# Performance work log

Hardware: AMD Instinct MI355X
Metric: run time of the kernel (lower is better)

The kernel has to match this reference:

```python
import jax, jax.numpy as jnp
import numpy as np

B, L, D = 16, 1024, 256  # batch, c_len == q_len (required by the expand/add in the source), 2*d_model


def mask_logits(x, m):
    # Faithful to the source's (unusual) masking: x*m + x*(1-m)*1e30
    return x * m + x * (1.0 - m) * 1e30


def setup_inputs() -> dict:
    key = jax.random.key(0)
    k = jax.random.split(key, 7)
    c = jax.random.normal(k[0], (B, L, D), dtype=jnp.float32)
    q = jax.random.normal(k[1], (B, L, D), dtype=jnp.float32)
    c_mask = jnp.ones((B, 1, L), dtype=jnp.float32)
    q_mask = jnp.ones((B, 1, L), dtype=jnp.float32)
    # Learned parameters (nn.Parameter zeros in the source; random here so the test is non-degenerate)
    c_weight = jax.random.normal(k[2], (D, 1), dtype=jnp.float32) * 0.05
    q_weight = jax.random.normal(k[3], (D, 1), dtype=jnp.float32) * 0.05
    cq_weight = jax.random.normal(k[4], (1, 1, D), dtype=jnp.float32) * 0.05
    bias = jnp.zeros((1,), dtype=jnp.float32)
    return {"c": c, "q": q, "c_mask": c_mask, "q_mask": q_mask,
            "c_weight": c_weight, "q_weight": q_weight,
            "cq_weight": cq_weight, "bias": bias}


def reference(c, q, c_mask, q_mask, c_weight, q_weight, cq_weight, bias):
    # Dropout treated as identity (inference) for a deterministic reference.
    s0 = jnp.matmul(c, c_weight)                      # [B, L, 1] -> broadcasts over q_len
    s1 = jnp.swapaxes(jnp.matmul(c, q_weight), 1, 2)  # [B, 1, L] (source uses c here, not q)
    s2 = jnp.einsum('bid,bjd->bij', c * cq_weight, q) # [B, L, L]
    S = s0 + s1 + s2 + bias                           # trilinear similarity
    S1 = jax.nn.softmax(mask_logits(S, q_mask), axis=-1)              # [B, Lc, Lq]
    C2Q = jnp.matmul(S1, q)                                           # [B, Lc, D]
    # torch F.softmax with no dim on a 3D tensor defaults to dim=0 (legacy behavior) -> axis=0
    S2 = jax.nn.softmax(mask_logits(jnp.swapaxes(S, 1, 2), c_mask), axis=0)  # [B, Lq, Lc]
    S2 = jnp.matmul(S1, S2)                                           # [B, Lc, Lc]
    Q2C = jnp.matmul(S2, c)                                           # [B, Lc, D]
    # torch.cat default dim=0 -> [4B, Lc, D]
    return jnp.concatenate((c, C2Q, c * C2Q, c * Q2C), axis=0)
```

## Files before the change

kernel.cpp:

```cpp
#include <hip/hip_runtime.h>

typedef __bf16 bf16;
typedef _Float16 f16;
typedef __attribute__((ext_vector_type(8))) __bf16 bf16x8;
typedef __attribute__((ext_vector_type(4))) __bf16 bf16x4;
typedef __attribute__((ext_vector_type(8))) _Float16 f16x8;
typedef __attribute__((ext_vector_type(4))) _Float16 f16x4;
typedef __attribute__((ext_vector_type(4))) float f32x4;

constexpr int Bn = 16, Ln = 1024, Dn = 256;

__device__ __forceinline__ float maskf(float m) { return m + (1.0f - m) * 1e30f; }

__device__ __forceinline__ void gload16(const void* g, void* l) {
  __builtin_amdgcn_global_load_lds((const __attribute__((address_space(1))) void*)g,
                                   (__attribute__((address_space(3))) void*)l, 16, 0, 0);
}

#define VMCNT(N) asm volatile("s_waitcnt vmcnt(" #N ")" ::: "memory")
#define LGKM0 asm volatile("s_waitcnt lgkmcnt(0)" ::: "memory")
#define BARR                                  \
  do {                                        \
    asm volatile("" ::: "memory");            \
    __builtin_amdgcn_s_barrier();             \
    asm volatile("" ::: "memory");            \
  } while (0)

__device__ __forceinline__ void stage512(const bf16* __restrict__ G, int ldg, int k0,
                                         bf16* L, int tid, int wid) {
#pragma unroll
  for (int p = 0; p < 2; ++p) {
    int u = tid + (p << 9);
    int row = u >> 3, s = u & 7;
    int kk = ((s ^ (row & 7)) << 3);
    gload16(G + (size_t)row * ldg + k0 + kk, L + ((p << 9) + (wid << 6)) * 8);
  }
}

__device__ __forceinline__ const bf16* swzp(const bf16* L, int row, int slot) {
  return L + row * 64 + ((slot ^ (row & 7)) << 3);
}

__global__ __launch_bounds__(256) void k_prep2(
    const float* __restrict__ c, const float* __restrict__ q,
    const float* __restrict__ cw, const float* __restrict__ qw,
    const float* __restrict__ cqw, bf16* __restrict__ cm, bf16* __restrict__ qb,
    bf16* __restrict__ cT, bf16* __restrict__ qT,
    float* __restrict__ s0, float* __restrict__ s1) {
  __shared__ __align__(16) bf16 tc[32][264];
  __shared__ __align__(16) bf16 tq[32][264];
  int blk = blockIdx.x;
  int b = blk >> 5;
  int l0 = (blk & 31) << 5;
  int t = threadIdx.x;
  int rl = t >> 3;
  int c0 = (t & 7) << 5;
  int grow = b * Ln + l0 + rl;
  size_t base = (size_t)grow * Dn + c0;
  float4 cv[8], qv[8];
#pragma unroll
  for (int k = 0; k < 8; ++k) {
    cv[k] = *(const float4*)&c[base + k * 4];
    qv[k] = *(const float4*)&q[base + k * 4];
  }
  float d0 = 0.f, d1 = 0.f;
#pragma unroll
  for (int k = 0; k < 8; ++k) {
    float4 w = *(const float4*)&cw[c0 + k * 4];
    float4 u = *(const float4*)&qw[c0 + k * 4];
    d0 += cv[k].x * w.x + cv[k].y * w.y + cv[k].z * w.z + cv[k].w * w.w;
    d1 += cv[k].x * u.x + cv[k].y * u.y + cv[k].z * u.z + cv[k].w * u.w;
  }
  d0 += __shfl_xor(d0, 1); d0 += __shfl_xor(d0, 2); d0 += __shfl_xor(d0, 4);
  d1 += __shfl_xor(d1, 1); d1 += __shfl_xor(d1, 2); d1 += __shfl_xor(d1, 4);
  if ((t & 7) == 0) { s0[grow] = d0; s1[grow] = d1; }
#pragma unroll
  for (int k2 = 0; k2 < 4; ++k2) {
    float4 m0 = *(const float4*)&cqw[c0 + k2 * 8];
    float4 m1 = *(const float4*)&cqw[c0 + k2 * 8 + 4];
    bf16x8 vm, vq, vc;
#pragma unroll
    for (int e = 0; e < 8; ++e) {
      float cvv = ((const float*)&cv[k2 * 2 + (e >> 2)])[e & 3];
      float qvv = ((const float*)&qv[k2 * 2 + (e >> 2)])[e & 3];
      float mw = (e < 4) ? ((const float*)&m0)[e] : ((const float*)&m1)[e - 4];
      vm[e] = (bf16)(cvv * mw);
      vq[e] = (bf16)qvv;
      vc[e] = (bf16)cvv;
    }
    *(bf16x8*)&cm[base + k2 * 8] = vm;
    *(bf16x8*)&qb[base + k2 * 8] = vq;
    *(bf16x8*)&tc[rl][c0 + k2 * 8] = vc;
    *(bf16x8*)&tq[rl][c0 + k2 * 8] = vq;
  }
  __syncthreads();
  int d = t;
  size_t tb = ((size_t)b * Dn + d) * Ln + l0;
  bf16x8 o[4];
#pragma unroll
  for (int j = 0; j < 4; ++j)
#pragma unroll
    for (int e = 0; e < 8; ++e) o[j][e] = tc[j * 8 + e][d];
#pragma unroll
  for (int j = 0; j < 4; ++j) *(bf16x8*)&cT[tb + j * 8] = o[j];
#pragma unroll
  for (int j = 0; j < 4; ++j)
#pragma unroll
    for (int e = 0; e < 8; ++e) o[j][e] = tq[j * 8 + e][d];
#pragma unroll
  for (int j = 0; j < 4; ++j) *(bf16x8*)&qT[tb + j * 8] = o[j];
}

__global__ __launch_bounds__(512) void g_s(const bf16* __restrict__ Am,
                                           const bf16* __restrict__ Bm,
                                           const float* __restrict__ s0,
                                           const float* __restrict__ s1,
                                           const float* __restrict__ bias,
                                           f16* __restrict__ S) {
  __shared__ __align__(16) bf16 lds[2][2 * 128 * 64];
  int f = blockIdx.x;
  int o = (f & 7) * 128 + (f >> 3);
  int bx = o & 7, by = (o >> 3) & 7, b = o >> 6;
  const bf16* Ab = Am + (size_t)b * Ln * Dn + (size_t)by * 128 * Dn;
  const bf16* Bb = Bm + (size_t)b * Ln * Dn + (size_t)bx * 128 * Dn;
  const int tid = threadIdx.x, wid = tid >> 6, lane = tid & 63;
  const int r = lane & 15, h = lane >> 4, wr = wid >> 2, wc = wid & 3;
  f32x4 acc[4][2];
  f32x4 zero = {0.f, 0.f, 0.f, 0.f};
#pragma unroll
  for (int i = 0; i < 4; ++i)
#pragma unroll
    for (int j = 0; j < 2; ++j) acc[i][j] = zero;

  stage512(Ab, Dn, 0, &lds[0][0], tid, wid);
  stage512(Bb, Dn, 0, &lds[0][8192], tid, wid);
  for (int t = 0; t < 4; ++t) {
    int cur = t & 1;
    if (t < 3) {
      stage512(Ab, Dn, (t + 1) * 64, &lds[cur ^ 1][0], tid, wid);
      stage512(Bb, Dn, (t + 1) * 64, &lds[cur ^ 1][8192], tid, wid);
      VMCNT(4);
    } else {
      VMCNT(0);
    }
    BARR;
    const bf16* lA = &lds[cur][0];
    const bf16* lB = &lds[cur][8192];
#pragma unroll
    for (int kk2 = 0; kk2 < 2; ++kk2) {
      int slot = (kk2 << 2) | h;
      bf16x8 av[4], bv[2];
#pragma unroll
      for (int i = 0; i < 4; ++i)
        av[i] = *(const bf16x8*)swzp(lA, (wr << 6) + (i << 4) + r, slot);
#pragma unroll
      for (int j = 0; j < 2; ++j)
        bv[j] = *(const bf16x8*)swzp(lB, (wc << 5) + (j << 4) + r, slot);
#pragma unroll
      for (int i = 0; i < 4; ++i)
#pragma unroll
        for (int j = 0; j < 2; ++j)
          acc[i][j] = __builtin_amdgcn_mfma_f32_16x16x32_bf16(av[i], bv[j], acc[i][j], 0, 0, 0);
    }
    LGKM0; BARR;
  }
  int grow = by * 128 + wr * 64, gcol = bx * 128 + wc * 32;
  float bvv = bias[0];
  size_t sb = (size_t)b * Ln * Ln;
#pragma unroll
  for (int j = 0; j < 2; ++j) {
    int n = gcol + j * 16 + r;
    float v1 = s1[b * Ln + n];
#pragma unroll
    for (int i = 0; i < 4; ++i) {
      int mb = grow + i * 16 + h * 4;
#pragma unroll
      for (int g = 0; g < 4; ++g) {
        float v0 = s0[b * Ln + mb + g];
        S[sb + (size_t)(mb + g) * Ln + n] = (f16)(acc[i][j][g] + v0 + v1 + bvv);
      }
    }
  }
}

__global__ __launch_bounds__(256) void k_sm(const f16* __restrict__ S,
                                            const float* __restrict__ qmask,
                                            const float* __restrict__ cmask,
                                            bf16* __restrict__ P1,
                                            bf16* __restrict__ P2) {
  __shared__ __align__(16) bf16 tile[16][32][36];
  int blk = blockIdx.x;
  int t = threadIdx.x;
  if (blk < 1024) {
    int i0 = (blk >> 5) << 5, j0 = (blk & 31) << 5;
    int ti = t >> 3, tj4 = (t & 7) << 2;
    int i = i0 + ti;
    const f16* Sp = S + (size_t)i * Ln + j0 + tj4;
    float fm[16];
#pragma unroll
    for (int b = 0; b < 16; ++b) fm[b] = maskf(cmask[b * Ln + i]);
    f16x4 u[16];
#pragma unroll
    for (int b = 0; b < 16; ++b) u[b] = *(const f16x4*)(Sp + (size_t)b * Ln * Ln);
    float m[4] = {-3.4e38f, -3.4e38f, -3.4e38f, -3.4e38f};
#pragma unroll
    for (int b = 0; b < 16; ++b)
#pragma unroll
      for (int g = 0; g < 4; ++g) m[g] = fmaxf(m[g], (float)u[b][g] * fm[b]);
    float e[16][4];
    float s[4] = {0.f, 0.f, 0.f, 0.f};
#pragma unroll
    for (int b = 0; b < 16; ++b)
#pragma unroll
      for (int g = 0; g < 4; ++g) {
        e[b][g] = __expf((float)u[b][g] * fm[b] - m[g]);
        s[g] += e[b][g];
      }
#pragma unroll
    for (int g = 0; g < 4; ++g) s[g] = 1.0f / s[g];
#pragma unroll
    for (int b = 0; b < 16; ++b)
#pragma unroll
      for (int g = 0; g < 4; ++g) tile[b][tj4 + g][ti] = (bf16)(e[b][g] * s[g]);
    __syncthreads();
    int jl = t >> 3, i4 = (t & 7) << 2;
#pragma unroll
    for (int b = 0; b < 16; ++b) {
      *(bf16x4*)&P2[((size_t)b * Ln + j0 + jl) * Ln + i0 + i4] =
          *(const bf16x4*)&tile[b][jl][i4];
    }
  } else {
    int row = (blk - 1024) * 4 + (t >> 6);
    int b = row >> 10;
    int lane = t & 63;
    const f16* Sr = S + (size_t)row * Ln;
    const float* qm = qmask + (size_t)b * Ln;
    float v[16];
    float mx = -3.4e38f;
#pragma unroll
    for (int p = 0; p < 2; ++p) {
      f16x8 x = ((const f16x8*)Sr)[lane + (p << 6)];
      float4 m0 = ((const float4*)qm)[(lane + (p << 6)) * 2];
      float4 m1 = ((const float4*)qm)[(lane + (p << 6)) * 2 + 1];
      float mm[8] = {m0.x, m0.y, m0.z, m0.w, m1.x, m1.y, m1.z, m1.w};
#pragma unroll
      for (int e = 0; e < 8; ++e) {
        float xv = (float)x[e] * maskf(mm[e]);
        v[8 * p + e] = xv;
        mx = fmaxf(mx, xv);
      }
    }
#pragma unroll
    for (int off = 32; off; off >>= 1) mx = fmaxf(mx, __shfl_xor(mx, off));
    float sum = 0.f;
#pragma unroll
    for (int k = 0; k < 16; ++k) {
      v[k] = __expf(v[k] - mx);
      sum += v[k];
    }
#pragma unroll
    for (int off = 32; off; off >>= 1) sum += __shfl_xor(sum, off);
    float inv = 1.0f / sum;
    bf16* Pr = P1 + (size_t)row * Ln;
#pragma unroll
    for (int p = 0; p < 2; ++p) {
      bf16x8 o;
#pragma unroll
      for (int e = 0; e < 8; ++e) o[e] = (bf16)(v[8 * p + e] * inv);
      ((bf16x8*)Pr)[lane + (p << 6)] = o;
    }
  }
}

__global__ __launch_bounds__(512) void g_t(const bf16* __restrict__ cT,
                                           const bf16* __restrict__ P2,
                                           bf16* __restrict__ TT) {
  __shared__ __align__(16) bf16 lds[2][2 * 128 * 64];
  int f = blockIdx.x;
  int o = (f & 7) * 32 + (f >> 3);
  int b = o >> 4, md = (o >> 3) & 1, nb = o & 7;
  const bf16* Ab = cT + (size_t)b * Dn * Ln + (size_t)md * 128 * Ln;
  const bf16* Bb = P2 + (size_t)b * Ln * Ln + (size_t)nb * 128 * Ln;
  const int tid = threadIdx.x, wid = tid >> 6, lane = tid & 63;
  const int r = lane & 15, h = lane >> 4, wr = wid >> 2, wc = wid & 3;
  f32x4 acc[4][2];
  f32x4 zero = {0.f, 0.f, 0.f, 0.f};
#pragma unroll
  for (int i = 0; i < 4; ++i)
#pragma unroll
    for (int j = 0; j < 2; ++j) acc[i][j] = zero;

  stage512(Ab, Ln, 0, &lds[0][0], tid, wid);
  stage512(Bb, Ln, 0, &lds[0][8192], tid, wid);
  for (int t = 0; t < 16; ++t) {
    int cur = t & 1;
    if (t < 15) {
      stage512(Ab, Ln, (t + 1) * 64, &lds[cur ^ 1][0], tid, wid);
      stage512(Bb, Ln, (t + 1) * 64, &lds[cur ^ 1][8192], tid, wid);
      VMCNT(4);
    } else {
      VMCNT(0);
    }
    BARR;
    const bf16* lA = &lds[cur][0];
    const bf16* lB = &lds[cur][8192];
#pragma unroll
    for (int kk2 = 0; kk2 < 2; ++kk2) {
      int slot = (kk2 << 2) | h;
      bf16x8 av[4], bv[2];
#pragma unroll
      for (int i = 0; i < 4; ++i)
        av[i] = *(const bf16x8*)swzp(lA, (wr << 6) + (i << 4) + r, slot);
#pragma unroll
      for (int j = 0; j < 2; ++j)
        bv[j] = *(const bf16x8*)swzp(lB, (wc << 5) + (j << 4) + r, slot);
#pragma unroll
      for (int i = 0; i < 4; ++i)
#pragma unroll
        for (int j = 0; j < 2; ++j)
          acc[i][j] = __builtin_amdgcn_mfma_f32_16x16x32_bf16(av[i], bv[j], acc[i][j], 0, 0, 0);
    }
    LGKM0; BARR;
  }
  size_t ob = (size_t)b * Dn * Ln;
  int dbase = md * 128 + wr * 64, cbase = nb * 128 + wc * 32;
#pragma unroll
  for (int i = 0; i < 4; ++i)
#pragma unroll
    for (int j = 0; j < 2; ++j) {
      int n = cbase + j * 16 + r;
#pragma unroll
      for (int g = 0; g < 4; ++g)
        TT[ob + (size_t)(dbase + i * 16 + h * 4 + g) * Ln + n] = (bf16)acc[i][j][g];
    }
}

__global__ __launch_bounds__(512) void g_cq(const bf16* __restrict__ P1,
                                            const bf16* __restrict__ qT,
                                            const bf16* __restrict__ TT,
                                            const float* __restrict__ c,
                                            float* __restrict__ out) {
  __shared__ __align__(16) bf16 lds[2][3 * 128 * 64];
  int f = blockIdx.x;
  int o = (f & 7) * 32 + (f >> 3);
  int b = o >> 4, by = (o >> 1) & 7, bx = o & 1;
  const bf16* Ab = P1 + (size_t)b * Ln * Ln + (size_t)by * 128 * Ln;
  const bf16* B1 = qT + (size_t)b * Dn * Ln + (size_t)bx * 128 * Ln;
  const bf16* B2 = TT + (size_t)b * Dn * Ln + (size_t)bx * 128 * Ln;
  const int tid = threadIdx.x, wid = tid >> 6, lane = tid & 63;
  const int r = lane & 15, h = lane >> 4, wr = wid >> 2, wc = wid & 3;
  f32x4 acc1[4][2], acc2[4][2];
  f32x4 zero = {0.f, 0.f, 0.f, 0.f};
#pragma unroll
  for (int i = 0; i < 4; ++i)
#pragma unroll
    for (int j = 0; j < 2; ++j) { acc1[i][j] = zero; acc2[i][j] = zero; }

  stage512(Ab, Ln, 0, &lds[0][0], tid, wid);
  stage512(B1, Ln, 0, &lds[0][8192], tid, wid);
  stage512(B2, Ln, 0, &lds[0][16384], tid, wid);
  for (int t = 0; t < 16; ++t) {
    int cur = t & 1;
    if (t < 15) {
      stage512(Ab, Ln, (t + 1) * 64, &lds[cur ^ 1][0], tid, wid);
      stage512(B1, Ln, (t + 1) * 64, &lds[cur ^ 1][8192], tid, wid);
      stage512(B2, Ln, (t + 1) * 64, &lds[cur ^ 1][16384], tid, wid);
      VMCNT(6);
    } else {
      VMCNT(0);
    }
    BARR;
    const bf16* lA = &lds[cur][0];
    const bf16* lB1 = &lds[cur][8192];
    const bf16* lB2 = &lds[cur][16384];
#pragma unroll
    for (int kk2 = 0; kk2 < 2; ++kk2) {
      int slot = (kk2 << 2) | h;
      bf16x8 av[4], bv[2];
#pragma unroll
      for (int i = 0; i < 4; ++i)
        av[i] = *(const bf16x8*)swzp(lA, (wr << 6) + (i << 4) + r, slot);
#pragma unroll
      for (int j = 0; j < 2; ++j)
        bv[j] = *(const bf16x8*)swzp(lB1, (wc << 5) + (j << 4) + r, slot);
#pragma unroll
      for (int i = 0; i < 4; ++i)
#pragma unroll
        for (int j = 0; j < 2; ++j)
          acc1[i][j] = __builtin_amdgcn_mfma_f32_16x16x32_bf16(av[i], bv[j], acc1[i][j], 0, 0, 0);
#pragma unroll
      for (int j = 0; j < 2; ++j)
        bv[j] = *(const bf16x8*)swzp(lB2, (wc << 5) + (j << 4) + r, slot);
#pragma unroll
      for (int i = 0; i < 4; ++i)
#pragma unroll
        for (int j = 0; j < 2; ++j)
          acc2[i][j] = __builtin_amdgcn_mfma_f32_16x16x32_bf16(av[i], bv[j], acc2[i][j], 0, 0, 0);
    }
    LGKM0; BARR;
  }

  int grow = by * 128 + wr * 64, gcol = bx * 128 + wc * 32;
  const float* cb = c + (size_t)b * Ln * Dn;
  float* o0 = out + (size_t)(0 * Bn + b) * Ln * Dn;
  float* o1 = out + (size_t)(1 * Bn + b) * Ln * Dn;
  float* o2 = out + (size_t)(2 * Bn + b) * Ln * Dn;
  float* o3 = out + (size_t)(3 * Bn + b) * Ln * Dn;
#pragma unroll
  for (int j = 0; j < 2; ++j) {
    int n = gcol + j * 16 + r;
#pragma unroll
    for (int i = 0; i < 4; ++i) {
      int mb = grow + i * 16 + h * 4;
#pragma unroll
      for (int g = 0; g < 4; ++g) {
        float v1 = acc1[i][j][g];
        float v2 = acc2[i][j][g];
        size_t off = (size_t)(mb + g) * Dn + n;
        float cc = cb[off];
        o0[off] = cc;
        o1[off] = v1;
        o2[off] = cc * v1;
        o3[off] = cc * v2;
      }
    }
  }
}

extern "C" void kernel_launch(void* const* d_in, const int* in_sizes, int n_in,
                              void* d_out, int out_size, void* d_ws, size_t ws_size,
                              hipStream_t stream) {
  const float* c = (const float*)d_in[0];
  const float* q = (const float*)d_in[1];
  const float* cmask = (const float*)d_in[2];
  const float* qmask = (const float*)d_in[3];
  const float* cw = (const float*)d_in[4];
  const float* qw = (const float*)d_in[5];
  const float* cqw = (const float*)d_in[6];
  const float* bias = (const float*)d_in[7];
  float* out = (float*)d_out;

  char* w = (char*)d_ws;
  f16* S = (f16*)w;       w += (size_t)Bn * Ln * Ln * 2;
  bf16* P1 = (bf16*)w;    w += (size_t)Bn * Ln * Ln * 2;
  bf16* P2 = (bf16*)w;    w += (size_t)Bn * Ln * Ln * 2;
  bf16* cm = (bf16*)w;    w += (size_t)Bn * Ln * Dn * 2;
  bf16* qb = (bf16*)w;    w += (size_t)Bn * Ln * Dn * 2;
  bf16* cT = (bf16*)w;    w += (size_t)Bn * Dn * Ln * 2;
  bf16* qT = (bf16*)w;    w += (size_t)Bn * Dn * Ln * 2;
  bf16* TT = (bf16*)w;    w += (size_t)Bn * Dn * Ln * 2;
  float* s0 = (float*)w;  w += (size_t)Bn * Ln * 4;
  float* s1 = (float*)w;  w += (size_t)Bn * Ln * 4;
  if ((size_t)(w - (char*)d_ws) > ws_size) return;

  k_prep2<<<dim3(Bn * Ln / 32), 256, 0, stream>>>(c, q, cw, qw, cqw, cm, qb, cT, qT, s0, s1);
  g_s<<<dim3(1024), 512, 0, stream>>>(cm, qb, s0, s1, bias, S);
  k_sm<<<dim3(1024 + Bn * Ln / 4), 256, 0, stream>>>(S, qmask, cmask, P1, P2);
  g_t<<<dim3(256), 512, 0, stream>>>(cT, P2, TT);
  g_cq<<<dim3(256), 512, 0, stream>>>(P1, qT, TT, c, out);
}
```

Before: 111.6 us.

## Triple-buffer g_cq LDS pipeline and halve k_sm transpose tile

The g_cq GEMM moves from double to triple buffering in LDS, prefetching two K-tiles ahead with matching vmcnt waits, so global loads have more time to land before they are consumed. In k_sm the transpose staging tile is halved, with the 16 batches written out in two passes of 8 and an extra barrier between them. This cuts k_sm's LDS footprint, likely to allow more resident blocks. g_cq's LDS use grows from about 96KB to 144KB per block, which may limit occupancy or exceed the per-CU LDS limit.

Measured after the change: 112.7 us. About the same (+1.0%).

```diff
diff --git a/kernel.cpp b/kernel.cpp
--- a/kernel.cpp
+++ b/kernel.cpp
@@ -188,7 +188,7 @@
                                             const float* __restrict__ cmask,
                                             bf16* __restrict__ P1,
                                             bf16* __restrict__ P2) {
-  __shared__ __align__(16) bf16 tile[16][32][36];
+  __shared__ __align__(16) bf16 tile[8][32][36];
   int blk = blockIdx.x;
   int t = threadIdx.x;
   if (blk < 1024) {
@@ -218,16 +218,22 @@
       }
 #pragma unroll
     for (int g = 0; g < 4; ++g) s[g] = 1.0f / s[g];
-#pragma unroll
-    for (int b = 0; b < 16; ++b)
-#pragma unroll
-      for (int g = 0; g < 4; ++g) tile[b][tj4 + g][ti] = (bf16)(e[b][g] * s[g]);
-    __syncthreads();
     int jl = t >> 3, i4 = (t & 7) << 2;
 #pragma unroll
-    for (int b = 0; b < 16; ++b) {
-      *(bf16x4*)&P2[((size_t)b * Ln + j0 + jl) * Ln + i0 + i4] =
-          *(const bf16x4*)&tile[b][jl][i4];
+    for (int half = 0; half < 2; ++half) {
+      if (half) __syncthreads();
+#pragma unroll
+      for (int bb = 0; bb < 8; ++bb) {
+        int b = half * 8 + bb;
+#pragma unroll
+        for (int g = 0; g < 4; ++g) tile[bb][tj4 + g][ti] = (bf16)(e[b][g] * s[g]);
+      }
+      __syncthreads();
+#pragma unroll
+      for (int bb = 0; bb < 8; ++bb) {
+        *(bf16x4*)&P2[((size_t)(half * 8 + bb) * Ln + j0 + jl) * Ln + i0 + i4] =
+            *(const bf16x4*)&tile[bb][jl][i4];
+      }
     }
   } else {
     int row = (blk - 1024) * 4 + (t >> 6);
@@ -340,7 +346,7 @@
                                             const bf16* __restrict__ TT,
                                             const float* __restrict__ c,
                                             float* __restrict__ out) {
-  __shared__ __align__(16) bf16 lds[2][3 * 128 * 64];
+  __shared__ __align__(16) bf16 lds[3][3 * 128 * 64];
   int f = blockIdx.x;
   int o = (f & 7) * 32 + (f >> 3);
   int b = o >> 4, by = (o >> 1) & 7, bx = o & 1;
@@ -359,12 +365,18 @@
   stage512(Ab, Ln, 0, &lds[0][0], tid, wid);
   stage512(B1, Ln, 0, &lds[0][8192], tid, wid);
   stage512(B2, Ln, 0, &lds[0][16384], tid, wid);
+  stage512(Ab, Ln, 64, &lds[1][0], tid, wid);
+  stage512(B1, Ln, 64, &lds[1][8192], tid, wid);
+  stage512(B2, Ln, 64, &lds[1][16384], tid, wid);
   for (int t = 0; t < 16; ++t) {
-    int cur = t & 1;
-    if (t < 15) {
-      stage512(Ab, Ln, (t + 1) * 64, &lds[cur ^ 1][0], tid, wid);
-      stage512(B1, Ln, (t + 1) * 64, &lds[cur ^ 1][8192], tid, wid);
-      stage512(B2, Ln, (t + 1) * 64, &lds[cur ^ 1][16384], tid, wid);
+    int cur = t % 3;
+    if (t < 14) {
+      int nxt = (t + 2) % 3;
+      stage512(Ab, Ln, (t + 2) * 64, &lds[nxt][0], tid, wid);
+      stage512(B1, Ln, (t + 2) * 64, &lds[nxt][8192], tid, wid);
+      stage512(B2, Ln, (t + 2) * 64, &lds[nxt][16384], tid, wid);
+      VMCNT(12);
+    } else if (t == 14) {
       VMCNT(6);
     } else {
       VMCNT(0);
```
